# Kernel optimization log

Hardware: AMD Instinct MI355X
Metric: run time of the kernel (lower is better)

The kernel has to match this reference:

```python
import jax, jax.numpy as jnp
import numpy as np

NUM_FEATURES = 1024
NUM_SAMPLES = 32768
BATCH = 4096
TEMP = 0.05
EPS = 1e-12


def setup_inputs() -> dict:
    key = jax.random.key(0)
    k1, k2, k3, k4 = jax.random.split(key, 4)
    inputs = jax.random.normal(k1, (BATCH, NUM_FEATURES), dtype=jnp.float32)
    targets = jax.random.randint(k2, (BATCH,), 0, NUM_SAMPLES, dtype=jnp.int64)
    corrected_targets = jax.random.randint(k3, (BATCH,), 0, NUM_SAMPLES, dtype=jnp.int64)
    # memory bank: buffer is zeros-initialized in torch, but in practice it is
    # filled with L2-normalized cluster centroids before use; emulate that.
    feats = jax.random.normal(k4, (NUM_SAMPLES, NUM_FEATURES), dtype=jnp.float32)
    feats = feats / jnp.linalg.norm(feats, axis=1, keepdims=True)
    return {"inputs": inputs, "targets": targets,
            "corrected_targets": corrected_targets, "features": feats}


def reference(inputs, targets, corrected_targets, features):
    # F.normalize(inputs, dim=1)
    x = inputs / jnp.maximum(jnp.linalg.norm(inputs, axis=1, keepdims=True), EPS)
    # CM.forward: inputs @ features.T, then / temp
    logits = jnp.einsum('bd,nd->bn', x, features) / TEMP  # [B, N]
    # F.cross_entropy(logits, corrected_targets, reduction='mean')
    logp = jax.nn.log_softmax(logits, axis=1)
    nll = -jnp.take_along_axis(logp, corrected_targets[:, None], axis=1)[:, 0]
    return jnp.mean(nll)
```

## Files before the change

### kernel.cpp

```cpp
#include <hip/hip_runtime.h>
#include <stdint.h>

#define B_ROWS 4096
#define N_FEAT 32768
#define K_DIM  1024
#define BM 256
#define BN 256
#define NT2 (N_FEAT / BN)

typedef __attribute__((ext_vector_type(8))) short bf16x8;
typedef __attribute__((ext_vector_type(4))) float f32x4;
typedef __attribute__((address_space(1))) unsigned char ga_u8;
typedef __attribute__((address_space(3))) unsigned char lds_u8;

__device__ inline unsigned short f2bf(float f) {
  union { float f; unsigned u; } v; v.f = f;
  unsigned r = v.u + 0x7FFF + ((v.u >> 16) & 1);
  return (unsigned short)(r >> 16);
}
__device__ inline float bf2f(unsigned short u) {
  union { unsigned u; float f; } v; v.u = ((unsigned)u) << 16;
  return v.f;
}

__global__ void k_prep(const float* __restrict__ in, unsigned short* __restrict__ xbf,
                       const float* __restrict__ f, unsigned short* __restrict__ fbf) {
  int bid = blockIdx.x;
  int t = threadIdx.x;
  if (bid < B_ROWS) {
    int row = bid;
    float4 v = reinterpret_cast<const float4*>(in + (size_t)row * K_DIM)[t];
    float ssq = v.x * v.x + v.y * v.y + v.z * v.z + v.w * v.w;
    #pragma unroll
    for (int d = 1; d < 64; d <<= 1) ssq += __shfl_xor(ssq, d);
    __shared__ float sm[4];
    if ((t & 63) == 0) sm[t >> 6] = ssq;
    __syncthreads();
    float nrm = sqrtf(sm[0] + sm[1] + sm[2] + sm[3]);
    float inv = 1.0f / fmaxf(nrm, 1e-12f);
    ushort4 o;
    o.x = f2bf(v.x * inv); o.y = f2bf(v.y * inv);
    o.z = f2bf(v.z * inv); o.w = f2bf(v.w * inv);
    reinterpret_cast<ushort4*>(xbf + (size_t)row * K_DIM)[t] = o;
  } else {
    const long n4 = (long)N_FEAT * K_DIM / 4;
    long i = (long)(bid - B_ROWS) * 256 + t;
    const long stride = 8192L * 256;
    for (; i < n4; i += stride) {
      float4 v = reinterpret_cast<const float4*>(f)[i];
      ushort4 o;
      o.x = f2bf(v.x); o.y = f2bf(v.y); o.z = f2bf(v.z); o.w = f2bf(v.w);
      reinterpret_cast<ushort4*>(fbf)[i] = o;
    }
  }
}

__global__ void k_tgt(const unsigned short* __restrict__ xbf,
                      const unsigned short* __restrict__ fbf,
                      const int* __restrict__ tgt, float* __restrict__ out) {
  int row = blockIdx.x * 4 + (threadIdx.x >> 6);
  int lane = threadIdx.x & 63;
  int t = tgt[row];
  const uint4* xa = reinterpret_cast<const uint4*>(xbf + (size_t)row * K_DIM + lane * 16);
  const uint4* fa = reinterpret_cast<const uint4*>(fbf + (size_t)t * K_DIM + lane * 16);
  float s = 0.f;
  #pragma unroll
  for (int j = 0; j < 2; ++j) {
    uint4 av = xa[j], fv = fa[j];
    const unsigned* ap = &av.x;
    const unsigned* fp = &fv.x;
    #pragma unroll
    for (int q = 0; q < 4; ++q) {
      s += bf2f((unsigned short)(ap[q] & 0xffff)) * bf2f((unsigned short)(fp[q] & 0xffff));
      s += bf2f((unsigned short)(ap[q] >> 16)) * bf2f((unsigned short)(fp[q] >> 16));
    }
  }
  #pragma unroll
  for (int d = 1; d < 64; d <<= 1) s += __shfl_xor(s, d);
  if (lane == 0) out[row] = s * 20.0f;
}


#define XSTR(s) STR(s)
#define STR(s) #s
#define WAITVN(N) asm volatile("s_waitcnt vmcnt(" XSTR(N) ")" ::: "memory")
#define LGKMN(N)  do { asm volatile("s_waitcnt lgkmcnt(" XSTR(N) ")" ::: "memory"); __builtin_amdgcn_sched_barrier(0); } while(0)
#define BAR       __builtin_amdgcn_s_barrier()
#define SCHED0    __builtin_amdgcn_sched_barrier(0)
#define PRIO1     __builtin_amdgcn_s_setprio(1)
#define PRIO0     __builtin_amdgcn_s_setprio(0)

__launch_bounds__(512, 2)
__global__ void k_gemm8(const unsigned short* __restrict__ xbf,
                        const unsigned short* __restrict__ fbf,
                        float* __restrict__ m_part, float* __restrict__ l_part) {
  __shared__ __align__(16) char lds_all[163840];
  char* ldsc = lds_all;

  int tid = threadIdx.x;
  int lane = tid & 63;
  int wid = tid >> 6;
  int wr = wid >> 2;
  int wc = wid & 3;
  int r15 = lane & 15;
  int g = lane >> 4;

  int bid = blockIdx.x;
  int swz = (bid & 7) * 256 + (bid >> 3);
  int mt = swz >> 7;
  int nt = swz & 127;
  int mBase = mt * BM, nBase = nt * BN;

  int lswz = ((g ^ ((r15 >> 1) & 3)) << 4);
  int aOff = (wr * 128 + r15) * 64 + lswz;
  int bOff = 16384 + (wc * 64 + r15) * 64 + lswz;

  int stRow = wid * 32 + (lane >> 2);
  int src_cb = (((lane & 3) ^ ((lane >> 3) & 3)) << 4);
  const char* srcA = (const char*)xbf + (size_t)(mBase + stRow) * (K_DIM * 2) + src_cb;
  const char* srcB = (const char*)fbf + (size_t)(nBase + stRow) * (K_DIM * 2) + src_cb;

#define STAGE5(SLOT, H) do { \
    const char* gA = srcA + (H) * 64; \
    char* dA = ldsc + (SLOT) * 32768 + wid * 2048; \
    __builtin_amdgcn_global_load_lds((const ga_u8*)gA, (lds_u8*)dA, 16, 0, 0); \
    __builtin_amdgcn_global_load_lds((const ga_u8*)(gA + 32768), (lds_u8*)(dA + 1024), 16, 0, 0); \
    const char* gB = srcB + (H) * 64; \
    char* dB = ldsc + (SLOT) * 32768 + 16384 + wid * 2048; \
    __builtin_amdgcn_global_load_lds((const ga_u8*)gB, (lds_u8*)dB, 16, 0, 0); \
    __builtin_amdgcn_global_load_lds((const ga_u8*)(gB + 32768), (lds_u8*)(dB + 1024), 16, 0, 0); \
  } while(0)

#define LDF(AA, BB, SLOT) do { \
    char* sb = ldsc + (SLOT) * 32768; \
    _Pragma("unroll") \
    for (int fm = 0; fm < 8; ++fm) \
      AA[fm] = *reinterpret_cast<const bf16x8*>(sb + aOff + fm * 1024); \
    _Pragma("unroll") \
    for (int fn = 0; fn < 4; ++fn) \
      BB[fn] = *reinterpret_cast<const bf16x8*>(sb + bOff + fn * 1024); \
  } while(0)

#define MM5(AA, BB) do { \
    _Pragma("unroll") \
    for (int fm = 0; fm < 8; ++fm) \
      _Pragma("unroll") \
      for (int fn = 0; fn < 4; ++fn) \
        acc[fm][fn] = __builtin_amdgcn_mfma_f32_16x16x32_bf16(AA[fm], BB[fn], acc[fm][fn], 0, 0, 0); \
  } while(0)

#define PHASE5(SNXT, SSTG, DOST, DOLD, VM, LG, ACUR, BCUR, ANXT, BNXT, H) do { \
    if (DOST) { STAGE5(SSTG, H); } \
    WAITVN(VM); \
    if (DOLD) { LDF(ANXT, BNXT, SNXT); } \
    LGKMN(LG); \
    PRIO1; MM5(ACUR, BCUR); PRIO0; \
    BAR; SCHED0; \
  } while(0)

#define PH_E(SNXT, SSTG, H) PHASE5(SNXT, SSTG, 1, 1, 8, 12, a0, b0, a1, b1, H)
#define PH_O(SNXT, SSTG, H) PHASE5(SNXT, SSTG, 1, 1, 8, 12, a1, b1, a0, b0, H)

  f32x4 acc[8][4];
  #pragma unroll
  for (int i = 0; i < 8; ++i)
    #pragma unroll
    for (int j = 0; j < 4; ++j)
      acc[i][j] = (f32x4){0.f, 0.f, 0.f, 0.f};
  bf16x8 a0[8], b0[4], a1[8], b1[4];

  STAGE5(0, 0); STAGE5(1, 1); STAGE5(2, 2); STAGE5(3, 3);
  WAITVN(8);
  BAR; SCHED0;
  LDF(a0, b0, 0);

  PH_E(1, 4, 4);   PH_O(2, 0, 5);   PH_E(3, 1, 6);   PH_O(4, 2, 7);   PH_E(0, 3, 8);
  PH_O(1, 4, 9);   PH_E(2, 0, 10);  PH_O(3, 1, 11);  PH_E(4, 2, 12);  PH_O(0, 3, 13);
  PH_E(1, 4, 14);  PH_O(2, 0, 15);  PH_E(3, 1, 16);  PH_O(4, 2, 17);  PH_E(0, 3, 18);
  PH_O(1, 4, 19);  PH_E(2, 0, 20);  PH_O(3, 1, 21);  PH_E(4, 2, 22);  PH_O(0, 3, 23);
  PH_E(1, 4, 24);  PH_O(2, 0, 25);  PH_E(3, 1, 26);  PH_O(4, 2, 27);  PH_E(0, 3, 28);
  PH_O(1, 4, 29);  PH_E(2, 0, 30);  PH_O(3, 1, 31);
  PHASE5(4, 0, 0, 1, 4, 12, a0, b0, a1, b1, 0);
  PHASE5(0, 0, 0, 1, 0, 12, a1, b1, a0, b0, 0);
  PHASE5(1, 0, 0, 1, 0, 12, a0, b0, a1, b1, 0);
  PHASE5(0, 0, 0, 0, 0, 0,  a1, b1, a0, b0, 0);

  asm volatile("s_waitcnt vmcnt(0) lgkmcnt(0)" ::: "memory");
  __syncthreads();
  float* sm_m = (float*)lds_all;
  float* sm_l = (float*)(lds_all + 4096);

  #pragma unroll
  for (int mf = 0; mf < 8; ++mf)
    #pragma unroll
    for (int fn = 0; fn < 4; ++fn)
      acc[mf][fn] = acc[mf][fn] * 20.0f;

  #pragma unroll
  for (int mf = 0; mf < 8; ++mf) {
    #pragma unroll
    for (int reg = 0; reg < 4; ++reg) {
      float mx = -1e30f;
      #pragma unroll
      for (int fn = 0; fn < 4; ++fn) mx = fmaxf(mx, acc[mf][fn][reg]);
      mx = fmaxf(mx, __shfl_xor(mx, 1));
      mx = fmaxf(mx, __shfl_xor(mx, 2));
      mx = fmaxf(mx, __shfl_xor(mx, 4));
      mx = fmaxf(mx, __shfl_xor(mx, 8));
      float sum = 0.f;
      #pragma unroll
      for (int fn = 0; fn < 4; ++fn) sum += __expf(acc[mf][fn][reg] - mx);
      sum += __shfl_xor(sum, 1);
      sum += __shfl_xor(sum, 2);
      sum += __shfl_xor(sum, 4);
      sum += __shfl_xor(sum, 8);
      if ((lane & 15) == 0) {
        int r = wr * 128 + mf * 16 + (lane >> 4) * 4 + reg;
        sm_m[wc * 256 + r] = mx;
        sm_l[wc * 256 + r] = sum;
      }
    }
  }
  __syncthreads();
  if (tid < 256) {
    float M = sm_m[tid], L = sm_l[tid];
    #pragma unroll
    for (int w = 1; w < 4; ++w) {
      float mo = sm_m[w * 256 + tid], lo = sm_l[w * 256 + tid];
      float mn = fmaxf(M, mo);
      L = L * __expf(M - mn) + lo * __expf(mo - mn);
      M = mn;
    }
    size_t idx = (size_t)(mBase + tid) * NT2 + nt;
    m_part[idx] = M;
    l_part[idx] = L;
  }
}

__global__ void k_comb(const float* __restrict__ m_part, const float* __restrict__ l_part,
                       const float* __restrict__ tgt_logit, float* __restrict__ nll) {
  int row = blockIdx.x;
  int lane = threadIdx.x;
  size_t base = (size_t)row * NT2;
  float m = m_part[base + lane];
  float l = l_part[base + lane];
  float m2 = m_part[base + 64 + lane];
  float l2 = l_part[base + 64 + lane];
  float mn = fmaxf(m, m2);
  l = l * __expf(m - mn) + l2 * __expf(m2 - mn);
  m = mn;
  #pragma unroll
  for (int d = 1; d < 64; d <<= 1) {
    float mo = __shfl_xor(m, d);
    float lo = __shfl_xor(l, d);
    float mx = fmaxf(m, mo);
    l = l * __expf(m - mx) + lo * __expf(mo - mx);
    m = mx;
  }
  if (lane == 0) nll[row] = m + __logf(l) - tgt_logit[row];
}

__global__ void k_mean(const float* __restrict__ nll, float* __restrict__ out) {
  int t = threadIdx.x;
  float s = 0.f;
  #pragma unroll
  for (int i = 0; i < 4; ++i) s += nll[t + i * 1024];
  #pragma unroll
  for (int d = 1; d < 64; d <<= 1) s += __shfl_xor(s, d);
  __shared__ float sm[16];
  if ((t & 63) == 0) sm[t >> 6] = s;
  __syncthreads();
  if (t == 0) {
    float tot = 0.f;
    #pragma unroll
    for (int w = 0; w < 16; ++w) tot += sm[w];
    out[0] = tot * (1.0f / B_ROWS);
  }
}

extern "C" void kernel_launch(void* const* d_in, const int* in_sizes, int n_in,
                              void* d_out, int out_size, void* d_ws, size_t ws_size,
                              hipStream_t stream) {
  const float* inputs = (const float*)d_in[0];
  const int* ctgt = (const int*)d_in[2];
  const float* feats = (const float*)d_in[3];
  float* out = (float*)d_out;

  char* ws = (char*)d_ws;
  unsigned short* xbf = (unsigned short*)ws;
  unsigned short* fbf = (unsigned short*)(ws + (8ull << 20));
  float* m_part = (float*)(ws + (72ull << 20));
  float* l_part = (float*)(ws + (74ull << 20));
  float* tgt_logit = (float*)(ws + (76ull << 20));
  float* nll = (float*)(ws + (76ull << 20) + (64ull << 10));

  k_prep<<<B_ROWS + 8192, 256, 0, stream>>>(inputs, xbf, feats, fbf);
  k_tgt<<<B_ROWS / 4, 256, 0, stream>>>(xbf, fbf, ctgt, tgt_logit);
  k_gemm8<<<(B_ROWS / BM) * (N_FEAT / BN), 512, 0, stream>>>(xbf, fbf, m_part, l_part);
  k_comb<<<B_ROWS, 64, 0, stream>>>(m_part, l_part, tgt_logit, nll);
  k_mean<<<1, 1024, 0, stream>>>(nll, out);
}
```

Measured before the change: 524.6 us.

## Switch GEMM to 32x32x16 MFMA with new LDS layout and fuse target logit

Replaces the 16x16x32 bf16 MFMA tiling with 32x32x16 MFMA, using a new global-to-LDS staging layout without the XOR swizzle and new fragment loads and accumulator indexing in the softmax epilogue. The target-logit dot product moves from a separate kernel into the combine kernel, and the partial max/sum buffers are transposed to column-major so combine reads are strided. The aim is fewer MFMA issues and LDS reads per tile plus one fewer launch. The risk is LDS bank conflicts from dropping the swizzle, and staging two 16B chunks per row may leave the K-slice layout mismatched with the fragment reads.

Measured after the change: 704.5 us. +34.3%, slower.

```diff
diff --git a/kernel.cpp b/kernel.cpp
--- a/kernel.cpp
+++ b/kernel.cpp
@@ -9,7 +9,7 @@
 #define NT2 (N_FEAT / BN)
 
 typedef __attribute__((ext_vector_type(8))) short bf16x8;
-typedef __attribute__((ext_vector_type(4))) float f32x4;
+typedef __attribute__((ext_vector_type(16))) float f32x16;
 typedef __attribute__((address_space(1))) unsigned char ga_u8;
 typedef __attribute__((address_space(3))) unsigned char lds_u8;
 
@@ -55,31 +55,6 @@
   }
 }
 
-__global__ void k_tgt(const unsigned short* __restrict__ xbf,
-                      const unsigned short* __restrict__ fbf,
-                      const int* __restrict__ tgt, float* __restrict__ out) {
-  int row = blockIdx.x * 4 + (threadIdx.x >> 6);
-  int lane = threadIdx.x & 63;
-  int t = tgt[row];
-  const uint4* xa = reinterpret_cast<const uint4*>(xbf + (size_t)row * K_DIM + lane * 16);
-  const uint4* fa = reinterpret_cast<const uint4*>(fbf + (size_t)t * K_DIM + lane * 16);
-  float s = 0.f;
-  #pragma unroll
-  for (int j = 0; j < 2; ++j) {
-    uint4 av = xa[j], fv = fa[j];
-    const unsigned* ap = &av.x;
-    const unsigned* fp = &fv.x;
-    #pragma unroll
-    for (int q = 0; q < 4; ++q) {
-      s += bf2f((unsigned short)(ap[q] & 0xffff)) * bf2f((unsigned short)(fp[q] & 0xffff));
-      s += bf2f((unsigned short)(ap[q] >> 16)) * bf2f((unsigned short)(fp[q] >> 16));
-    }
-  }
-  #pragma unroll
-  for (int d = 1; d < 64; d <<= 1) s += __shfl_xor(s, d);
-  if (lane == 0) out[row] = s * 20.0f;
-}
-
 
 #define XSTR(s) STR(s)
 #define STR(s) #s
@@ -102,8 +77,6 @@
   int wid = tid >> 6;
   int wr = wid >> 2;
   int wc = wid & 3;
-  int r15 = lane & 15;
-  int g = lane >> 4;
 
   int bid = blockIdx.x;
   int swz = (bid & 7) * 256 + (bid >> 3);
@@ -111,42 +84,48 @@
   int nt = swz & 127;
   int mBase = mt * BM, nBase = nt * BN;
 
-  int lswz = ((g ^ ((r15 >> 1) & 3)) << 4);
-  int aOff = (wr * 128 + r15) * 64 + lswz;
-  int bOff = 16384 + (wc * 64 + r15) * 64 + lswz;
-
-  int stRow = wid * 32 + (lane >> 2);
-  int src_cb = (((lane & 3) ^ ((lane >> 3) & 3)) << 4);
-  const char* srcA = (const char*)xbf + (size_t)(mBase + stRow) * (K_DIM * 2) + src_cb;
-  const char* srcB = (const char*)fbf + (size_t)(nBase + stRow) * (K_DIM * 2) + src_cb;
+  const char* srcA = (const char*)xbf + (size_t)(mBase + wid * 32 + (lane & 31)) * (K_DIM * 2)
+                     + ((lane >> 5) * 16);
+  const char* srcB = (const char*)fbf + (size_t)(nBase + wid * 32 + (lane & 31)) * (K_DIM * 2)
+                     + ((lane >> 5) * 16);
+
+  char* aBase = ldsc + lane * 16 + wr * 8192;
+  char* bBase = ldsc + lane * 16 + 16384 + wc * 4096;
 
 #define STAGE5(SLOT, H) do { \
     const char* gA = srcA + (H) * 64; \
     char* dA = ldsc + (SLOT) * 32768 + wid * 2048; \
     __builtin_amdgcn_global_load_lds((const ga_u8*)gA, (lds_u8*)dA, 16, 0, 0); \
-    __builtin_amdgcn_global_load_lds((const ga_u8*)(gA + 32768), (lds_u8*)(dA + 1024), 16, 0, 0); \
+    __builtin_amdgcn_global_load_lds((const ga_u8*)(gA + 32), (lds_u8*)(dA + 1024), 16, 0, 0); \
     const char* gB = srcB + (H) * 64; \
     char* dB = ldsc + (SLOT) * 32768 + 16384 + wid * 2048; \
     __builtin_amdgcn_global_load_lds((const ga_u8*)gB, (lds_u8*)dB, 16, 0, 0); \
-    __builtin_amdgcn_global_load_lds((const ga_u8*)(gB + 32768), (lds_u8*)(dB + 1024), 16, 0, 0); \
+    __builtin_amdgcn_global_load_lds((const ga_u8*)(gB + 32), (lds_u8*)(dB + 1024), 16, 0, 0); \
   } while(0)
 
 #define LDF(AA, BB, SLOT) do { \
-    char* sb = ldsc + (SLOT) * 32768; \
+    char* sa = aBase + (SLOT) * 32768; \
     _Pragma("unroll") \
-    for (int fm = 0; fm < 8; ++fm) \
-      AA[fm] = *reinterpret_cast<const bf16x8*>(sb + aOff + fm * 1024); \
+    for (int mf = 0; mf < 4; ++mf) \
+      _Pragma("unroll") \
+      for (int ks = 0; ks < 2; ++ks) \
+        AA[mf][ks] = *reinterpret_cast<const bf16x8*>(sa + (mf * 2 + ks) * 1024); \
+    char* sb = bBase + (SLOT) * 32768; \
     _Pragma("unroll") \
-    for (int fn = 0; fn < 4; ++fn) \
-      BB[fn] = *reinterpret_cast<const bf16x8*>(sb + bOff + fn * 1024); \
+    for (int nf = 0; nf < 2; ++nf) \
+      _Pragma("unroll") \
+      for (int ks = 0; ks < 2; ++ks) \
+        BB[nf][ks] = *reinterpret_cast<const bf16x8*>(sb + (nf * 2 + ks) * 1024); \
   } while(0)
 
 #define MM5(AA, BB) do { \
     _Pragma("unroll") \
-    for (int fm = 0; fm < 8; ++fm) \
+    for (int ks = 0; ks < 2; ++ks) \
       _Pragma("unroll") \
-      for (int fn = 0; fn < 4; ++fn) \
-        acc[fm][fn] = __builtin_amdgcn_mfma_f32_16x16x32_bf16(AA[fm], BB[fn], acc[fm][fn], 0, 0, 0); \
+      for (int mf = 0; mf < 4; ++mf) \
+        _Pragma("unroll") \
+        for (int nf = 0; nf < 2; ++nf) \
+          acc[mf][nf] = __builtin_amdgcn_mfma_f32_32x32x16_bf16(AA[mf][ks], BB[nf][ks], acc[mf][nf], 0, 0, 0); \
   } while(0)
 
 #define PHASE5(SNXT, SSTG, DOST, DOLD, VM, LG, ACUR, BCUR, ANXT, BNXT, H) do { \
@@ -161,13 +140,15 @@
 #define PH_E(SNXT, SSTG, H) PHASE5(SNXT, SSTG, 1, 1, 8, 12, a0, b0, a1, b1, H)
 #define PH_O(SNXT, SSTG, H) PHASE5(SNXT, SSTG, 1, 1, 8, 12, a1, b1, a0, b0, H)
 
-  f32x4 acc[8][4];
-  #pragma unroll
-  for (int i = 0; i < 8; ++i)
-    #pragma unroll
-    for (int j = 0; j < 4; ++j)
-      acc[i][j] = (f32x4){0.f, 0.f, 0.f, 0.f};
-  bf16x8 a0[8], b0[4], a1[8], b1[4];
+  f32x16 acc[4][2];
+  #pragma unroll
+  for (int i = 0; i < 4; ++i)
+    #pragma unroll
+    for (int j = 0; j < 2; ++j)
+      #pragma unroll
+      for (int r = 0; r < 16; ++r)
+        acc[i][j][r] = 0.f;
+  bf16x8 a0[4][2], b0[2][2], a1[4][2], b1[2][2];
 
   STAGE5(0, 0); STAGE5(1, 1); STAGE5(2, 2); STAGE5(3, 3);
   WAITVN(8);
@@ -191,31 +172,30 @@
   float* sm_l = (float*)(lds_all + 4096);
 
   #pragma unroll
-  for (int mf = 0; mf < 8; ++mf)
-    #pragma unroll
-    for (int fn = 0; fn < 4; ++fn)
-      acc[mf][fn] = acc[mf][fn] * 20.0f;
-
-  #pragma unroll
-  for (int mf = 0; mf < 8; ++mf) {
-    #pragma unroll
-    for (int reg = 0; reg < 4; ++reg) {
-      float mx = -1e30f;
-      #pragma unroll
-      for (int fn = 0; fn < 4; ++fn) mx = fmaxf(mx, acc[mf][fn][reg]);
+  for (int mf = 0; mf < 4; ++mf)
+    #pragma unroll
+    for (int nf = 0; nf < 2; ++nf)
+      acc[mf][nf] = acc[mf][nf] * 20.0f;
+
+  #pragma unroll
+  for (int mf = 0; mf < 4; ++mf) {
+    #pragma unroll
+    for (int reg = 0; reg < 16; ++reg) {
+      float mx = fmaxf(acc[mf][0][reg], acc[mf][1][reg]);
       mx = fmaxf(mx, __shfl_xor(mx, 1));
       mx = fmaxf(mx, __shfl_xor(mx, 2));
       mx = fmaxf(mx, __shfl_xor(mx, 4));
       mx = fmaxf(mx, __shfl_xor(mx, 8));
-      float sum = 0.f;
-      #pragma unroll
-      for (int fn = 0; fn < 4; ++fn) sum += __expf(acc[mf][fn][reg] - mx);
+      mx = fmaxf(mx, __shfl_xor(mx, 16));
+      float sum = __expf(acc[mf][0][reg] - mx) + __expf(acc[mf][1][reg] - mx);
       sum += __shfl_xor(sum, 1);
       sum += __shfl_xor(sum, 2);
       sum += __shfl_xor(sum, 4);
       sum += __shfl_xor(sum, 8);
-      if ((lane & 15) == 0) {
-        int r = wr * 128 + mf * 16 + (lane >> 4) * 4 + reg;
+      sum += __shfl_xor(sum, 16);
+      if ((lane & 31) == 0) {
+        int rl = (reg & 3) + 8 * (reg >> 2) + 4 * (lane >> 5);
+        int r = wr * 128 + mf * 32 + rl;
         sm_m[wc * 256 + r] = mx;
         sm_l[wc * 256 + r] = sum;
       }
@@ -231,21 +211,41 @@
       L = L * __expf(M - mn) + lo * __expf(mo - mn);
       M = mn;
     }
-    size_t idx = (size_t)(mBase + tid) * NT2 + nt;
+    size_t idx = (size_t)nt * B_ROWS + (mBase + tid);
     m_part[idx] = M;
     l_part[idx] = L;
   }
 }
 
 __global__ void k_comb(const float* __restrict__ m_part, const float* __restrict__ l_part,
-                       const float* __restrict__ tgt_logit, float* __restrict__ nll) {
+                       const unsigned short* __restrict__ xbf,
+                       const unsigned short* __restrict__ fbf,
+                       const int* __restrict__ tgt, float* __restrict__ nll) {
   int row = blockIdx.x;
   int lane = threadIdx.x;
-  size_t base = (size_t)row * NT2;
-  float m = m_part[base + lane];
-  float l = l_part[base + lane];
-  float m2 = m_part[base + 64 + lane];
-  float l2 = l_part[base + 64 + lane];
+
+  int t = tgt[row];
+  const uint4* xa = reinterpret_cast<const uint4*>(xbf + (size_t)row * K_DIM + lane * 16);
+  const uint4* fa = reinterpret_cast<const uint4*>(fbf + (size_t)t * K_DIM + lane * 16);
+  float s = 0.f;
+  #pragma unroll
+  for (int j = 0; j < 2; ++j) {
+    uint4 av = xa[j], fv = fa[j];
+    const unsigned* ap = &av.x;
+    const unsigned* fp = &fv.x;
+    #pragma unroll
+    for (int q = 0; q < 4; ++q) {
+      s += bf2f((unsigned short)(ap[q] & 0xffff)) * bf2f((unsigned short)(fp[q] & 0xffff));
+      s += bf2f((unsigned short)(ap[q] >> 16)) * bf2f((unsigned short)(fp[q] >> 16));
+    }
+  }
+  #pragma unroll
+  for (int d = 1; d < 64; d <<= 1) s += __shfl_xor(s, d);
+
+  float m = m_part[(size_t)lane * B_ROWS + row];
+  float l = l_part[(size_t)lane * B_ROWS + row];
+  float m2 = m_part[(size_t)(lane + 64) * B_ROWS + row];
+  float l2 = l_part[(size_t)(lane + 64) * B_ROWS + row];
   float mn = fmaxf(m, m2);
   l = l * __expf(m - mn) + l2 * __expf(m2 - mn);
   m = mn;
@@ -257,7 +257,7 @@
     l = l * __expf(m - mx) + lo * __expf(mo - mx);
     m = mx;
   }
-  if (lane == 0) nll[row] = m + __logf(l) - tgt_logit[row];
+  if (lane == 0) nll[row] = m + __logf(l) - s * 20.0f;
 }
 
 __global__ void k_mean(const float* __restrict__ nll, float* __restrict__ out) {
@@ -291,12 +291,10 @@
   unsigned short* fbf = (unsigned short*)(ws + (8ull << 20));
   float* m_part = (float*)(ws + (72ull << 20));
   float* l_part = (float*)(ws + (74ull << 20));
-  float* tgt_logit = (float*)(ws + (76ull << 20));
-  float* nll = (float*)(ws + (76ull << 20) + (64ull << 10));
+  float* nll = (float*)(ws + (76ull << 20));
 
   k_prep<<<B_ROWS + 8192, 256, 0, stream>>>(inputs, xbf, feats, fbf);
-  k_tgt<<<B_ROWS / 4, 256, 0, stream>>>(xbf, fbf, ctgt, tgt_logit);
   k_gemm8<<<(B_ROWS / BM) * (N_FEAT / BN), 512, 0, stream>>>(xbf, fbf, m_part, l_part);
-  k_comb<<<B_ROWS, 64, 0, stream>>>(m_part, l_part, tgt_logit, nll);
+  k_comb<<<B_ROWS, 64, 0, stream>>>(m_part, l_part, xbf, fbf, ctgt, nll);
   k_mean<<<1, 1024, 0, stream>>>(nll, out);
 }
```
